# Performance work log

Hardware: AMD Instinct MI355X
Metric: run time of the kernel (lower is better)

The kernel has to match this reference:

```python
import jax, jax.numpy as jnp
import numpy as np

N_NODES = 50000
N_EDGES = 1600000
IN_DIM = 128
OUT_DIM = 64
HEADS = 4
NEG_SLOPE = 0.2


def setup_inputs() -> dict:
    key = jax.random.key(0)
    ks = jax.random.split(key, 6)
    x = jax.random.normal(ks[0], (N_NODES, IN_DIM), dtype=jnp.float32)
    edge_index = jax.random.randint(ks[1], (2, N_EDGES), 0, N_NODES, dtype=jnp.int64)
    scale = 1.0 / np.sqrt(IN_DIM)
    W = jax.random.normal(ks[2], (IN_DIM, HEADS * OUT_DIM), dtype=jnp.float32) * scale
    att_src = jax.random.normal(ks[3], (HEADS, OUT_DIM), dtype=jnp.float32) * scale
    att_dst = jax.random.normal(ks[4], (HEADS, OUT_DIM), dtype=jnp.float32) * scale
    bias = jnp.zeros((HEADS * OUT_DIM,), dtype=jnp.float32)
    return {"x": x, "edge_index": edge_index, "W": W, "att_src": att_src, "att_dst": att_dst, "bias": bias}


def reference(x, edge_index, W, att_src, att_dst, bias):
    N = x.shape[0]
    H, F = att_src.shape
    # PyG GATConv default: add self-loops (static shape: E + N edges)
    loops = jnp.arange(N, dtype=edge_index.dtype)
    ei = jnp.concatenate([edge_index, jnp.stack([loops, loops])], axis=1)
    src, dst = ei[0], ei[1]
    # linear projection, split heads: [N, H, F]
    h = (x @ W).reshape(N, H, F)
    # per-node attention logits per head: [N, H]
    a_s = jnp.einsum('nhf,hf->nh', h, att_src)
    a_d = jnp.einsum('nhf,hf->nh', h, att_dst)
    # per-edge score: gather + LeakyReLU -> [E, H]
    e = jax.nn.leaky_relu(a_s[src] + a_d[dst], negative_slope=NEG_SLOPE)
    # segment softmax over incoming edges of each dst node
    m = jax.ops.segment_max(e, dst, num_segments=N)
    ex = jnp.exp(e - m[dst])
    s = jax.ops.segment_sum(ex, dst, num_segments=N)
    alpha = ex / (s[dst] + 1e-16)
    # weighted message scatter-aggregate: [N, H, F]
    msg = h[src] * alpha[:, :, None]
    out = jax.ops.segment_sum(msg, dst, num_segments=N)
    return out.reshape(N, H * F) + bias
```

## Files before the change

kernel.cpp:

```cpp
#include <hip/hip_runtime.h>

constexpr int N_NODES = 50000;
constexpr int N_EDGES = 1600000;
constexpr int E_TOT   = N_EDGES + N_NODES;
constexpr int IN_DIM  = 128;
constexpr int HEADS   = 4;
constexpr int FDIM    = 64;
constexpr int HF      = 256;
constexpr float NEG   = 0.2f;
constexpr int NB_SCAN = (N_NODES + 255) / 256;

__device__ __forceinline__ float leaky(float t) {
    return fmaxf(t, 0.f) + NEG * fminf(t, 0.f);
}

__device__ __forceinline__ unsigned short f2bf(float f) {
    unsigned int u = __float_as_uint(f);
    u += 0x7fffu + ((u >> 16) & 1u);
    return (unsigned short)(u >> 16);
}
__device__ __forceinline__ float bf_lo(unsigned int u) {
    return __uint_as_float(u << 16);
}
__device__ __forceinline__ float bf_hi(unsigned int u) {
    return __uint_as_float(u & 0xffff0000u);
}

__device__ __forceinline__ int wave_incl_scan(int v, int lane) {
    #pragma unroll
    for (int off = 1; off < 64; off <<= 1) {
        int n = __shfl_up(v, off);
        if (lane >= off) v += n;
    }
    return v;
}

__global__ __launch_bounds__(256) void gemm_kernel(const float* __restrict__ x,
                                                   const float* __restrict__ W,
                                                   const float* __restrict__ att_src,
                                                   const float* __restrict__ att_dst,
                                                   unsigned short* __restrict__ h_bf,
                                                   float* __restrict__ a_s,
                                                   float* __restrict__ a_d) {
    __shared__ float xs[IN_DIM][64];
    const int t = threadIdx.x;
    const int node0 = blockIdx.x * 64;

    {
        const int r  = t & 63;
        const int k0 = (t >> 6) * 32;
        int row = node0 + r;
        if (row >= N_NODES) row = N_NODES - 1;
        const float4* src = reinterpret_cast<const float4*>(&x[row * IN_DIM + k0]);
        #pragma unroll
        for (int i = 0; i < 8; ++i) {
            float4 v = src[i];
            int k = k0 + i * 4;
            xs[k + 0][r] = v.x;
            xs[k + 1][r] = v.y;
            xs[k + 2][r] = v.z;
            xs[k + 3][r] = v.w;
        }
    }
    __syncthreads();

    const int l  = t & 63;
    const int c  = l * 4;
    const int rg = (t >> 6) * 16;
    float acc[16][4];
    #pragma unroll
    for (int r = 0; r < 16; ++r)
        #pragma unroll
        for (int j = 0; j < 4; ++j) acc[r][j] = 0.f;

    #pragma unroll 2
    for (int k = 0; k < IN_DIM; ++k) {
        const float4 wv = *reinterpret_cast<const float4*>(&W[k * HF + c]);
        const float4 xa = *reinterpret_cast<const float4*>(&xs[k][rg + 0]);
        const float4 xb = *reinterpret_cast<const float4*>(&xs[k][rg + 4]);
        const float4 xc = *reinterpret_cast<const float4*>(&xs[k][rg + 8]);
        const float4 xd = *reinterpret_cast<const float4*>(&xs[k][rg + 12]);
        const float xr[16] = {xa.x, xa.y, xa.z, xa.w, xb.x, xb.y, xb.z, xb.w,
                              xc.x, xc.y, xc.z, xc.w, xd.x, xd.y, xd.z, xd.w};
        #pragma unroll
        for (int r = 0; r < 16; ++r) {
            acc[r][0] = fmaf(xr[r], wv.x, acc[r][0]);
            acc[r][1] = fmaf(xr[r], wv.y, acc[r][1]);
            acc[r][2] = fmaf(xr[r], wv.z, acc[r][2]);
            acc[r][3] = fmaf(xr[r], wv.w, acc[r][3]);
        }
    }

    const float4 asv = *reinterpret_cast<const float4*>(&att_src[c]);
    const float4 adv = *reinterpret_cast<const float4*>(&att_dst[c]);
    #pragma unroll
    for (int r = 0; r < 16; ++r) {
        float ps = acc[r][0] * asv.x + acc[r][1] * asv.y +
                   acc[r][2] * asv.z + acc[r][3] * asv.w;
        float pd = acc[r][0] * adv.x + acc[r][1] * adv.y +
                   acc[r][2] * adv.z + acc[r][3] * adv.w;
        #pragma unroll
        for (int off = 1; off < 16; off <<= 1) {
            ps += __shfl_xor(ps, off);
            pd += __shfl_xor(pd, off);
        }
        const int node = node0 + rg + r;
        if ((l & 15) == 0 && node < N_NODES) {
            a_s[node * HEADS + (l >> 4)] = ps;
            a_d[node * HEADS + (l >> 4)] = pd;
        }
    }

    #pragma unroll
    for (int r = 0; r < 16; ++r) {
        const int node = node0 + rg + r;
        if (node < N_NODES) {
            ushort4 v;
            v.x = f2bf(acc[r][0]); v.y = f2bf(acc[r][1]);
            v.z = f2bf(acc[r][2]); v.w = f2bf(acc[r][3]);
            *reinterpret_cast<ushort4*>(&h_bf[node * HF + c]) = v;
        }
    }
}

__global__ void zero_kernel(int* __restrict__ counts) {
    const int i = blockIdx.x * blockDim.x + threadIdx.x;
    if (i < N_NODES) counts[i] = 0;
}

__global__ void hist_kernel(const int* __restrict__ ei, int* __restrict__ counts) {
    const int e = blockIdx.x * blockDim.x + threadIdx.x;
    if (e >= E_TOT) return;
    const int dst = (e < N_EDGES) ? ei[N_EDGES + e] : e - N_EDGES;
    atomicAdd(&counts[dst], 1);
}

__global__ __launch_bounds__(256) void scanA_kernel(const int* __restrict__ counts,
                                                    int* __restrict__ local,
                                                    int* __restrict__ bsum) {
    const int t = threadIdx.x, lane = t & 63, w = t >> 6;
    const int i = blockIdx.x * 256 + t;
    const int v = (i < N_NODES) ? counts[i] : 0;
    const int inc = wave_incl_scan(v, lane);
    __shared__ int wt[4];
    if (lane == 63) wt[w] = inc;
    __syncthreads();
    int base = 0;
    #pragma unroll
    for (int k = 0; k < 3; ++k) if (k < w) base += wt[k];
    if (i < N_NODES) local[i] = base + inc - v;
    if (t == 255) bsum[blockIdx.x] = base + inc;
}

__global__ __launch_bounds__(256) void scanB_kernel(const int* __restrict__ bsum,
                                                    int* __restrict__ boff) {
    const int t = threadIdx.x, lane = t & 63, w = t >> 6;
    const int v = (t < NB_SCAN) ? bsum[t] : 0;
    const int inc = wave_incl_scan(v, lane);
    __shared__ int wt[4];
    if (lane == 63) wt[w] = inc;
    __syncthreads();
    int base = 0;
    #pragma unroll
    for (int k = 0; k < 3; ++k) if (k < w) base += wt[k];
    if (t < NB_SCAN) boff[t] = base + inc - v;
}

__global__ __launch_bounds__(256) void scanC_kernel(const int* __restrict__ local,
                                                    const int* __restrict__ boff,
                                                    int* __restrict__ offsets,
                                                    int* __restrict__ cursor) {
    const int i = blockIdx.x * 256 + threadIdx.x;
    if (i < N_NODES) {
        const int o = local[i] + boff[blockIdx.x];
        offsets[i] = o;
        cursor[i]  = o;
    }
    if (i == 0) offsets[N_NODES] = E_TOT;
}

__global__ void fill_kernel(const int* __restrict__ ei,
                            int* __restrict__ cursor,
                            int* __restrict__ sorted_src) {
    const int e = blockIdx.x * blockDim.x + threadIdx.x;
    if (e >= E_TOT) return;
    int src, dst;
    if (e < N_EDGES) { src = ei[e]; dst = ei[N_EDGES + e]; }
    else             { src = dst = e - N_EDGES; }
    const int slot = atomicAdd(&cursor[dst], 1);
    sorted_src[slot] = src;
}

__global__ __launch_bounds__(256) void gather_kernel(const int* __restrict__ sorted_src,
                                                     const float* __restrict__ a_s,
                                                     const float* __restrict__ a_d,
                                                     const int* __restrict__ offsets,
                                                     const unsigned short* __restrict__ h_bf,
                                                     const float* __restrict__ bias,
                                                     float* __restrict__ out) {
    const int dst  = (blockIdx.x * 256 + threadIdx.x) >> 6;
    const int lane = threadIdx.x & 63;
    if (dst >= N_NODES) return;
    const int half = lane >> 5;
    const int il   = lane & 31;
    const int hd   = il >> 3;

    const int beg = __builtin_amdgcn_readfirstlane(offsets[dst]);
    const int end = __builtin_amdgcn_readfirstlane(offsets[dst + 1]);
    const float ad = a_d[dst * HEADS + hd];

    float a0 = 0.f, a1 = 0.f, a2 = 0.f, a3 = 0.f;
    float a4 = 0.f, a5 = 0.f, a6 = 0.f, a7 = 0.f;
    float dsum = 0.f;

    auto body = [&](int slot) {
        const int   src = sorted_src[slot];
        const float as  = a_s[src * HEADS + hd];
        const float ex  = expf(leaky(as + ad));
        const uint4 hv  = *reinterpret_cast<const uint4*>(&h_bf[src * HF + il * 8]);
        a0 = fmaf(ex, bf_lo(hv.x), a0); a1 = fmaf(ex, bf_hi(hv.x), a1);
        a2 = fmaf(ex, bf_lo(hv.y), a2); a3 = fmaf(ex, bf_hi(hv.y), a3);
        a4 = fmaf(ex, bf_lo(hv.z), a4); a5 = fmaf(ex, bf_hi(hv.z), a5);
        a6 = fmaf(ex, bf_lo(hv.w), a6); a7 = fmaf(ex, bf_hi(hv.w), a7);
        dsum += ex;
    };

    int j = beg;
    for (; j + 7 < end; j += 8) {
        body(j + half);
        body(j + 2 + half);
        body(j + 4 + half);
        body(j + 6 + half);
    }
    for (; j + 1 < end; j += 2) body(j + half);
    if (j < end && half == 0) body(j);

    a0 += __shfl_xor(a0, 32); a1 += __shfl_xor(a1, 32);
    a2 += __shfl_xor(a2, 32); a3 += __shfl_xor(a3, 32);
    a4 += __shfl_xor(a4, 32); a5 += __shfl_xor(a5, 32);
    a6 += __shfl_xor(a6, 32); a7 += __shfl_xor(a7, 32);
    dsum += __shfl_xor(dsum, 32);

    const float inv = 1.f / (dsum + 1e-16f);
    const int eo = il * 8 + half * 4;
    const float4 bv = *reinterpret_cast<const float4*>(&bias[eo]);
    float4 o;
    o.x = (half ? a4 : a0) * inv + bv.x;
    o.y = (half ? a5 : a1) * inv + bv.y;
    o.z = (half ? a6 : a2) * inv + bv.z;
    o.w = (half ? a7 : a3) * inv + bv.w;
    *reinterpret_cast<float4*>(&out[dst * HF + eo]) = o;
}

extern "C" void kernel_launch(void* const* d_in, const int* in_sizes, int n_in,
                              void* d_out, int out_size, void* d_ws, size_t ws_size,
                              hipStream_t stream) {
    const float* x       = (const float*)d_in[0];
    const int*   ei      = (const int*)d_in[1];
    const float* W       = (const float*)d_in[2];
    const float* att_src = (const float*)d_in[3];
    const float* att_dst = (const float*)d_in[4];
    const float* bias    = (const float*)d_in[5];
    float* out = (float*)d_out;

    char* ws = (char*)d_ws;
    unsigned short* h_bf = (unsigned short*)(ws);
    float*  a_s        = (float*) (ws + 25600000);
    float*  a_d        = (float*) (ws + 26400000);
    int*    counts     = (int*)   (ws + 27200000);
    int*    offsets    = (int*)   (ws + 27400000);
    int*    cursor     = (int*)   (ws + 27600016);
    int*    sorted_src = (int*)   (ws + 27800016);
    int*    local      = (int*)   (ws + 34400016);
    int*    bsum       = (int*)   (ws + 34600016);
    int*    boff       = (int*)   (ws + 34600800);

    gemm_kernel<<<(N_NODES + 63) / 64, 256, 0, stream>>>(x, W, att_src, att_dst,
                                                         h_bf, a_s, a_d);
    zero_kernel<<<(N_NODES + 255) / 256, 256, 0, stream>>>(counts);
    hist_kernel<<<(E_TOT + 255) / 256, 256, 0, stream>>>(ei, counts);
    scanA_kernel<<<NB_SCAN, 256, 0, stream>>>(counts, local, bsum);
    scanB_kernel<<<1, 256, 0, stream>>>(bsum, boff);
    scanC_kernel<<<NB_SCAN, 256, 0, stream>>>(local, boff, offsets, cursor);
    fill_kernel<<<(E_TOT + 255) / 256, 256, 0, stream>>>(ei, cursor, sorted_src);
    const long total_threads = (long)N_NODES * 64;
    gather_kernel<<<(int)((total_threads + 255) / 256), 256, 0, stream>>>(
        sorted_src, a_s, a_d, offsets, h_bf, bias, out);
}
```

Measured before the change: 475.6 us.

## Record per-edge rank in histogram and fill CSR without second atomic pass

The histogram kernel now stores the atomic return value as each edge's rank within its destination, so the fill kernel can compute its slot as offsets[dst]+rank without a second round of atomics. The fill is split into 8 destination-range partitions per edge chunk, so each block writes only to a localized region of sorted_src, aiming for better L2/MALL write locality. The cost is a 6.6 MB rank array written and re-read, plus reading the dst array eight times in the fill.

```diff
diff --git a/kernel.cpp b/kernel.cpp
--- a/kernel.cpp
+++ b/kernel.cpp
@@ -9,6 +9,9 @@
 constexpr int HF      = 256;
 constexpr float NEG   = 0.2f;
 constexpr int NB_SCAN = (N_NODES + 255) / 256;
+constexpr int NPX     = (N_NODES + 7) / 8;
+constexpr int FILL_CH = 16384;
+constexpr int FILL_K  = (E_TOT + FILL_CH - 1) / FILL_CH;
 
 __device__ __forceinline__ float leaky(float t) {
     return fmaxf(t, 0.f) + NEG * fminf(t, 0.f);
@@ -128,11 +131,13 @@
     if (i < N_NODES) counts[i] = 0;
 }
 
-__global__ void hist_kernel(const int* __restrict__ ei, int* __restrict__ counts) {
+__global__ void hist_kernel(const int* __restrict__ ei,
+                            int* __restrict__ counts,
+                            int* __restrict__ rank) {
     const int e = blockIdx.x * blockDim.x + threadIdx.x;
     if (e >= E_TOT) return;
     const int dst = (e < N_EDGES) ? ei[N_EDGES + e] : e - N_EDGES;
-    atomicAdd(&counts[dst], 1);
+    rank[e] = atomicAdd(&counts[dst], 1);
 }
 
 __global__ __launch_bounds__(256) void scanA_kernel(const int* __restrict__ counts,
@@ -168,27 +173,28 @@
 
 __global__ __launch_bounds__(256) void scanC_kernel(const int* __restrict__ local,
                                                     const int* __restrict__ boff,
-                                                    int* __restrict__ offsets,
-                                                    int* __restrict__ cursor) {
+                                                    int* __restrict__ offsets) {
     const int i = blockIdx.x * 256 + threadIdx.x;
-    if (i < N_NODES) {
-        const int o = local[i] + boff[blockIdx.x];
-        offsets[i] = o;
-        cursor[i]  = o;
-    }
+    if (i < N_NODES) offsets[i] = local[i] + boff[blockIdx.x];
     if (i == 0) offsets[N_NODES] = E_TOT;
 }
 
-__global__ void fill_kernel(const int* __restrict__ ei,
-                            int* __restrict__ cursor,
-                            int* __restrict__ sorted_src) {
-    const int e = blockIdx.x * blockDim.x + threadIdx.x;
-    if (e >= E_TOT) return;
-    int src, dst;
-    if (e < N_EDGES) { src = ei[e]; dst = ei[N_EDGES + e]; }
-    else             { src = dst = e - N_EDGES; }
-    const int slot = atomicAdd(&cursor[dst], 1);
-    sorted_src[slot] = src;
+__global__ __launch_bounds__(256) void fill_kernel(const int* __restrict__ ei,
+                                                   const int* __restrict__ rank,
+                                                   const int* __restrict__ offsets,
+                                                   int* __restrict__ sorted_src) {
+    const int bid = blockIdx.x;
+    const int lo  = (bid & 7) * NPX;
+    const int hi  = min(N_NODES, lo + NPX);
+    const int e0  = (bid >> 3) * FILL_CH;
+    const int e1  = min(E_TOT, e0 + FILL_CH);
+    for (int e = e0 + threadIdx.x; e < e1; e += 256) {
+        const int dst = (e < N_EDGES) ? ei[N_EDGES + e] : e - N_EDGES;
+        if (dst >= lo && dst < hi) {
+            const int src = (e < N_EDGES) ? ei[e] : dst;
+            sorted_src[offsets[dst] + rank[e]] = src;
+        }
+    }
 }
 
 __global__ __launch_bounds__(256) void gather_kernel(const int* __restrict__ sorted_src,
@@ -269,20 +275,20 @@
     float*  a_d        = (float*) (ws + 26400000);
     int*    counts     = (int*)   (ws + 27200000);
     int*    offsets    = (int*)   (ws + 27400000);
-    int*    cursor     = (int*)   (ws + 27600016);
-    int*    sorted_src = (int*)   (ws + 27800016);
-    int*    local      = (int*)   (ws + 34400016);
-    int*    bsum       = (int*)   (ws + 34600016);
-    int*    boff       = (int*)   (ws + 34600800);
+    int*    rank       = (int*)   (ws + 27600016);
+    int*    sorted_src = (int*)   (ws + 34200016);
+    int*    local      = (int*)   (ws + 40800016);
+    int*    bsum       = (int*)   (ws + 41000016);
+    int*    boff       = (int*)   (ws + 41000800);
 
     gemm_kernel<<<(N_NODES + 63) / 64, 256, 0, stream>>>(x, W, att_src, att_dst,
                                                          h_bf, a_s, a_d);
     zero_kernel<<<(N_NODES + 255) / 256, 256, 0, stream>>>(counts);
-    hist_kernel<<<(E_TOT + 255) / 256, 256, 0, stream>>>(ei, counts);
+    hist_kernel<<<(E_TOT + 255) / 256, 256, 0, stream>>>(ei, counts, rank);
     scanA_kernel<<<NB_SCAN, 256, 0, stream>>>(counts, local, bsum);
     scanB_kernel<<<1, 256, 0, stream>>>(bsum, boff);
-    scanC_kernel<<<NB_SCAN, 256, 0, stream>>>(local, boff, offsets, cursor);
-    fill_kernel<<<(E_TOT + 255) / 256, 256, 0, stream>>>(ei, cursor, sorted_src);
+    scanC_kernel<<<NB_SCAN, 256, 0, stream>>>(local, boff, offsets);
+    fill_kernel<<<8 * FILL_K, 256, 0, stream>>>(ei, rank, offsets, sorted_src);
     const long total_threads = (long)N_NODES * 64;
     gather_kernel<<<(int)((total_threads + 255) / 256), 256, 0, stream>>>(
         sorted_src, a_s, a_d, offsets, h_bf, bias, out);
```

New measurement: 392.9 us. 17.4% less time.
